# Performance work log

Hardware: AMD Instinct MI355X
Metric: run time of the kernel (lower is better)

## Reference

```python
import jax, jax.numpy as jnp
import numpy as np

B, N, C, E, O = 4, 128, 256, 128, 128
NEG = -1.0e9


def setup_inputs() -> dict:
    key = jax.random.key(0)
    ks = jax.random.split(key, 24)
    s = jnp.float32(0.02)
    w = lambda k, shp: jax.random.normal(k, shp, jnp.float32) * s
    mm = jax.random.randint(ks[3], (B, N, N), 0, 2).astype(bool)
    return {
        "z": jax.random.normal(ks[0], (B, N, C), jnp.float32),
        "e": jax.random.normal(ks[1], (B, N, N, E), jnp.float32),
        "g": jax.random.normal(ks[2], (B, C // 2), jnp.float32),
        "mask": jnp.ones((B, N), bool),
        "msgs_mask": mm | jnp.eye(N, dtype=bool)[None],  # ensure each max-col nonempty
        "Wt1": w(ks[4], (C, 8)), "Wt2": w(ks[5], (C, 8)), "Wt3": w(ks[6], (C, 8)),
        "Wte1": w(ks[7], (E, 8)), "Wte2": w(ks[8], (E, 8)), "Wte3": w(ks[9], (E, 8)),
        "Wtg": w(ks[10], (C // 2, 8)),
        "Wm1": w(ks[11], (C, O)), "Wm2": w(ks[12], (C, O)),
        "Wme": w(ks[13], (E, O)), "Wmg": w(ks[14], (C // 2, O)),
        "Wmlp1": w(ks[15], (O, O)), "Wmlp2": w(ks[16], (O, O)),
        "WU1": w(ks[17], (C, O)), "WU2": w(ks[18], (O, O)), "WU3": w(ks[19], (8, O)),
    }


def reference(z, e, g, mask, msgs_mask, Wt1, Wt2, Wt3, Wte1, Wte2, Wte3, Wtg,
              Wm1, Wm2, Wme, Wmg, Wmlp1, Wmlp2, WU1, WU2, WU3):
    m = mask[..., None]  # (B,N,1)
    # --- triplet path ---
    t1 = jnp.where(m, z @ Wt1, 0.0)  # (B,N,8)
    t2 = jnp.where(m, z @ Wt2, 0.0)
    t3 = jnp.where(m, z @ Wt3, 0.0)
    te1 = e @ Wte1  # (B,N,N,8)
    te2 = e @ Wte2
    te3 = e @ Wte3
    tg = g @ Wtg  # (B,8)
    # (B,N,N,N,8) 7-way broadcast sum
    tri = (t1[:, :, None, None, :] + t2[:, None, :, None, :] + t3[:, None, None, :, :]
           + te1[:, :, :, None, :] + te2[:, :, None, :, :] + te3[:, None, :, :, :]
           + tg[:, None, None, None, :])
    msk_tri = mask[:, None, None, :] | mask[:, None, :, None] | mask[:, :, None, None]
    tri = jnp.where(msk_tri[..., None], tri, NEG)
    tri_msgs = jnp.max(tri, axis=1) @ WU3  # (B,N,N,O)
    # --- pairwise message path ---
    m1 = jnp.where(m, z @ Wm1, 0.0)  # (B,N,O)
    m2 = jnp.where(m, z @ Wm2, 0.0)
    me = jnp.where(msgs_mask[..., None], e @ Wme, 0.0)  # (B,N,N,O)
    mg = g @ Wmg  # (B,O)
    msgs = m1[:, None, :, :] + m2[:, :, None, :] + me + mg[:, None, None, :]
    msgs = jax.nn.relu(msgs) @ Wmlp1  # num_layers=2 MLP: (ReLU,Lin)x2
    msgs = jax.nn.relu(msgs) @ Wmlp2
    msgs = jnp.where(msgs_mask[..., None], msgs, NEG)
    msgs = jnp.max(msgs, axis=1)  # (B,N,O)
    ret = z @ WU1 + msgs @ WU2
    return (ret, msgs, tri_msgs)
```

## Files before the change

kernel.cpp:

```cpp
#include <hip/hip_runtime.h>
#include <hip/hip_bf16.h>
#include <cstdint>
#include <cstddef>

namespace {

constexpr int B = 4, N = 128, C = 256, E = 128, O = 128, CH = 8;
constexpr float NEGV = -1.0e9f;

constexpr size_t SZ_TE_F  = (size_t)B * N * N * CH / 2;
constexpr size_t OFF_TE1T = 0;
constexpr size_t OFF_TE2  = OFF_TE1T + SZ_TE_F;
constexpr size_t OFF_TE3  = OFF_TE2 + SZ_TE_F;
constexpr size_t OFF_M1   = OFF_TE3 + SZ_TE_F;
constexpr size_t OFF_M2   = OFF_M1 + (size_t)B * N * O;
constexpr size_t OFF_ZU1  = OFF_M2 + (size_t)B * N * O;
constexpr size_t OFF_T1   = OFF_ZU1 + (size_t)B * N * O;
constexpr size_t OFF_T2   = OFF_T1 + (size_t)B * N * CH;
constexpr size_t OFF_T3   = OFF_T2 + (size_t)B * N * CH;
constexpr size_t OFF_TG   = OFF_T3 + (size_t)B * N * CH;
constexpr size_t OFF_WT   = OFF_TG + (size_t)B * CH;
constexpr size_t OFF_PART = OFF_WT + (size_t)3 * O * E / 2;

typedef __attribute__((ext_vector_type(4))) float f32x4;
typedef __attribute__((ext_vector_type(8))) short bf16x8;
typedef __attribute__((ext_vector_type(8))) unsigned short u16x8;
typedef __attribute__((ext_vector_type(4))) unsigned u32x4;

__device__ __forceinline__ unsigned short f2b(float f) {
  unsigned u = __float_as_uint(f);
  u = (u + 0x7fffu + ((u >> 16) & 1u)) >> 16;
  return (unsigned short)u;
}
__device__ __forceinline__ float b2f(unsigned short u) {
  return __uint_as_float((unsigned)u << 16);
}

}

__global__ __launch_bounds__(256) void k_prep(
    const float* __restrict__ z, const float* __restrict__ g,
    const float* __restrict__ e,
    const float* __restrict__ Wt1, const float* __restrict__ Wt2,
    const float* __restrict__ Wt3, const float* __restrict__ Wtg,
    const float* __restrict__ Wm1, const float* __restrict__ Wm2,
    const float* __restrict__ Wmg, const float* __restrict__ WU1,
    const float* __restrict__ Wte1, const float* __restrict__ Wte2,
    const float* __restrict__ Wte3,
    const float* __restrict__ Wme, const float* __restrict__ Wmlp1,
    const float* __restrict__ Wmlp2, float* __restrict__ ws) {
  __shared__ __align__(16) char smem[17408];
  const int blk = blockIdx.x;
  const int t = threadIdx.x;

  if (blk < 512) {
    unsigned short* wpack = (unsigned short*)(smem);
    unsigned short* outl  = (unsigned short*)(smem + 8704);
    unsigned short* te1T = (unsigned short*)(ws + OFF_TE1T);
    unsigned short* te2  = (unsigned short*)(ws + OFF_TE2);
    unsigned short* te3  = (unsigned short*)(ws + OFF_TE3);
    const int b = blk >> 7, i = blk & 127;

    for (int x = t; x < 3072; x += 256) {
      const int m = x >> 10, rem = x & 1023, k = rem >> 3, c = rem & 7;
      const float* W = (m == 0) ? Wte1 : ((m == 1) ? Wte2 : Wte3);
      const int row = m * 8 + c;
      wpack[row * 136 + k] = f2b(W[rem]);
    }
    for (int x = t; x < 1024; x += 256) {
      const int row = 24 + (x >> 7), col = x & 127;
      wpack[row * 136 + col] = 0;
    }
    __syncthreads();

    const float* erow = e + ((size_t)(b * N) + i) * N * E;
    const int lane = t & 63, wid = t >> 6;
    const int li = lane & 15, lk8 = (lane >> 4) * 8, lq4 = (lane >> 4) * 4;
    const int jt = wid & 1, ct = wid >> 1;
    const int c0 = ct * 16 + lq4;

    bf16x8 wf[4];
#pragma unroll
    for (int kt = 0; kt < 4; ++kt) {
      const int rw = ct * 16 + li;
      wf[kt] = *reinterpret_cast<const bf16x8*>(&wpack[rw * 136 + kt * 32 + lk8]);
    }

#pragma unroll 2
    for (int step = 0; step < 4; ++step) {
      const int jrow = step * 32 + jt * 16 + li;
      const float* er = erow + (size_t)jrow * E;
      float4 v[4][2];
#pragma unroll
      for (int kt = 0; kt < 4; ++kt) {
        v[kt][0] = *reinterpret_cast<const float4*>(&er[kt * 32 + lk8]);
        v[kt][1] = *reinterpret_cast<const float4*>(&er[kt * 32 + lk8 + 4]);
      }
      f32x4 acc = {0.f, 0.f, 0.f, 0.f};
#pragma unroll
      for (int kt = 0; kt < 4; ++kt) {
        u16x8 af;
        af[0] = f2b(v[kt][0].x); af[1] = f2b(v[kt][0].y);
        af[2] = f2b(v[kt][0].z); af[3] = f2b(v[kt][0].w);
        af[4] = f2b(v[kt][1].x); af[5] = f2b(v[kt][1].y);
        af[6] = f2b(v[kt][1].z); af[7] = f2b(v[kt][1].w);
        acc = __builtin_amdgcn_mfma_f32_16x16x32_bf16(
            wf[kt], (bf16x8)af, acc, 0, 0, 0);
      }
      if (c0 < 24) {
        ushort4 pk;
        pk.x = f2b(acc[0]); pk.y = f2b(acc[1]);
        pk.z = f2b(acc[2]); pk.w = f2b(acc[3]);
        *reinterpret_cast<ushort4*>(&outl[jrow * 32 + c0]) = pk;
      }
    }
    __syncthreads();
    for (int x = t; x < 384; x += 256) {
      const int m = x >> 7, j = x & 127;
      const u16x8 v = *reinterpret_cast<const u16x8*>(&outl[j * 32 + m * 8]);
      if (m == 0)
        *reinterpret_cast<u16x8*>(&te1T[(((size_t)(b * N) + j) * N + i) * CH]) = v;
      else if (m == 1)
        *reinterpret_cast<u16x8*>(&te2[(((size_t)(b * N) + i) * N + j) * CH]) = v;
      else
        *reinterpret_cast<u16x8*>(&te3[(((size_t)(b * N) + i) * N + j) * CH]) = v;
    }
  } else if (blk < 1024) {
    float* zrow = (float*)(smem);
    float* grow = (float*)(smem + 1024);
    const int bn = blk - 512;
    const int b = bn >> 7, n = bn & 127;

    for (int k = t; k < C; k += 256) zrow[k] = z[((size_t)(b * N) + n) * C + k];
    if (t < C / 2) grow[t] = g[(size_t)b * (C / 2) + t];
    __syncthreads();

    {
      const int o = t & 127;
      const float* W = (t < 128) ? Wm1 : Wm2;
      float acc = 0.f;
#pragma unroll 16
      for (int k = 0; k < C; ++k) acc += zrow[k] * W[(size_t)k * O + o];
      if (t < 128) {
        float mgacc = 0.f;
#pragma unroll 8
        for (int k = 0; k < C / 2; ++k) mgacc += grow[k] * Wmg[(size_t)k * O + o];
        acc += mgacc;
        ws[OFF_M1 + ((size_t)(b * N) + n) * O + o] = acc;
      } else {
        ws[OFF_M2 + ((size_t)(b * N) + n) * O + o] = acc;
      }
    }
    if (t < 128) {
      float acc = 0.f;
#pragma unroll 16
      for (int k = 0; k < C; ++k) acc += zrow[k] * WU1[(size_t)k * O + t];
      ws[OFF_ZU1 + ((size_t)(b * N) + n) * O + t] = acc;
    } else if (t < 152) {
      const int idx = t - 128;
      const int which = idx >> 3, c = idx & 7;
      const float* W = (which == 0) ? Wt1 : ((which == 1) ? Wt2 : Wt3);
      float acc = 0.f;
#pragma unroll 8
      for (int k = 0; k < C; ++k) acc += zrow[k] * W[(size_t)k * CH + c];
      const size_t off = (which == 0) ? OFF_T1 : ((which == 1) ? OFF_T2 : OFF_T3);
      ws[off + ((size_t)(b * N) + n) * CH + c] = acc;
    }
    if (n == 0 && t >= 152 && t < 160) {
      const int c = t - 152;
      float acc = 0.f;
      for (int k = 0; k < C / 2; ++k) acc += grow[k] * Wtg[(size_t)k * CH + c];
      ws[OFF_TG + (size_t)b * CH + c] = acc;
    }
  } else {
    const int which = blk - 1024;
    const float* W = (which == 0) ? Wme : ((which == 1) ? Wmlp1 : Wmlp2);
    unsigned short* dst = (unsigned short*)(ws + OFF_WT) + (size_t)which * O * E;
    for (int x = t; x < O * E; x += 256) {
      const int o = x >> 7, k = x & 127;
      dst[x] = f2b(W[(size_t)k * O + o]);
    }
  }
}

__global__ __launch_bounds__(512) void k_main(
    const float* __restrict__ e, const void* __restrict__ msk,
    const float* __restrict__ WU3, const float* __restrict__ ws_c,
    float* __restrict__ ws, float* __restrict__ out_tri) {
  __shared__ __align__(16) char smem[34816];
  const int blk = blockIdx.x;
  const int t = threadIdx.x;

  if (blk < 256) {
    unsigned short* lds_w = (unsigned short*)smem;
    const int b = blk >> 6, jp = blk & 63;
    const int j0 = jp * 2;
    const int lane = t & 63, wid = t >> 6;
    const int li = lane & 15, g = lane >> 4;
    const int i = wid * 16 + li;

    int fmt;
    {
      const unsigned w = ((const unsigned*)msk)[lane];
      const float f = __uint_as_float(w);
      const unsigned long long bi = __ballot(w > 1u);
      const unsigned long long bfl = __ballot(!(f == 0.f || f == 1.f));
      fmt = (bi == 0ull) ? 0 : ((bfl == 0ull) ? 2 : 1);
    }
    int mkv0, mkv1;
    {
      const size_t ia = ((size_t)(b * N) + i) * N + j0;
      const size_t ib = ia + 1;
      if (fmt == 0) { mkv0 = ((const int*)msk)[ia] != 0; mkv1 = ((const int*)msk)[ib] != 0; }
      else if (fmt == 1) { mkv0 = ((const unsigned char*)msk)[ia] != 0; mkv1 = ((const unsigned char*)msk)[ib] != 0; }
      else { mkv0 = ((const float*)msk)[ia] != 0.f; mkv1 = ((const float*)msk)[ib] != 0.f; }
    }

    float4 m2r[8];
#pragma unroll
    for (int ot = 0; ot < 8; ++ot)
      m2r[ot] = *reinterpret_cast<const float4*>(
          &ws_c[OFF_M2 + ((size_t)(b * N) + i) * O + ot * 16 + g * 4]);

    bf16x8 bfrag[2][4];
#pragma unroll
    for (int jj = 0; jj < 2; ++jj)
#pragma unroll
      for (int kt = 0; kt < 4; ++kt) {
        const float* ep =
            &e[(((size_t)(b * N) + i) * N + j0 + jj) * E + kt * 32 + g * 8];
        const float4 v0 = *reinterpret_cast<const float4*>(ep);
        const float4 v1 = *reinterpret_cast<const float4*>(ep + 4);
        u16x8 af;
        af[0] = f2b(v0.x); af[1] = f2b(v0.y); af[2] = f2b(v0.z); af[3] = f2b(v0.w);
        af[4] = f2b(v1.x); af[5] = f2b(v1.y); af[6] = f2b(v1.z); af[7] = f2b(v1.w);
        bfrag[jj][kt] = (bf16x8)af;
      }

    f32x4 acc[2][8];
    const unsigned short* wts = (const unsigned short*)(ws_c + OFF_WT);

#define STAGE_W(L)                                                        \
  { const unsigned short* wl = wts + (size_t)(L)*O * E;                   \
    _Pragma("unroll") for (int x = 0; x < 4; ++x) {                       \
      const int idx = t + x * 512;                                        \
      const int row = idx >> 4, cg = idx & 15;                            \
      *reinterpret_cast<u16x8*>(&lds_w[row * 136 + cg * 8]) =             \
          *reinterpret_cast<const u16x8*>(&wl[row * 128 + cg * 8]);       \
    } }

#define MFMA_L()                                                          \
  _Pragma("unroll") for (int ot = 0; ot < 8; ++ot) {                      \
    acc[0][ot] = (f32x4){0.f, 0.f, 0.f, 0.f};                             \
    acc[1][ot] = (f32x4){0.f, 0.f, 0.f, 0.f};                             \
    _Pragma("unroll") for (int kt = 0; kt < 4; ++kt) {                    \
      const bf16x8 wf = *reinterpret_cast<const bf16x8*>(                 \
          &lds_w[(ot * 16 + li) * 136 + kt * 32 + g * 8]);                \
      acc[0][ot] = __builtin_amdgcn_mfma_f32_16x16x32_bf16(               \
          wf, bfrag[0][kt], acc[0][ot], 0, 0, 0);                         \
      acc[1][ot] = __builtin_amdgcn_mfma_f32_16x16x32_bf16(               \
          wf, bfrag[1][kt], acc[1][ot], 0, 0, 0);                         \
    } }

#define TRANSITION(jj)                                                    \
  { unsigned pk0[8], pk1[8];                                              \
    _Pragma("unroll") for (int ot = 0; ot < 8; ++ot) {                    \
      pk0[ot] = (unsigned)f2b(acc[jj][ot][0]) |                           \
                ((unsigned)f2b(acc[jj][ot][1]) << 16);                    \
      pk1[ot] = (unsigned)f2b(acc[jj][ot][2]) |                           \
                ((unsigned)f2b(acc[jj][ot][3]) << 16);                    \
    }                                                                     \
    const int src1 = ((lane >> 4) & 1) * 32 + li;                         \
    const int src2 = src1 + 16;                                           \
    const bool hi = lane >= 32;                                           \
    _Pragma("unroll") for (int kt = 0; kt < 4; ++kt) {                    \
      const unsigned a0 = __shfl(pk0[2 * kt], src1);                      \
      const unsigned b0 = __shfl(pk0[2 * kt + 1], src1);                  \
      const unsigned a1 = __shfl(pk1[2 * kt], src1);                      \
      const unsigned b1 = __shfl(pk1[2 * kt + 1], src1);                  \
      const unsigned a2 = __shfl(pk0[2 * kt], src2);                      \
      const unsigned b2 = __shfl(pk0[2 * kt + 1], src2);                  \
      const unsigned a3 = __shfl(pk1[2 * kt], src2);                      \
      const unsigned b3 = __shfl(pk1[2 * kt + 1], src2);                  \
      u32x4 q;                                                            \
      q.x = hi ? b0 : a0; q.y = hi ? b1 : a1;                             \
      q.z = hi ? b2 : a2; q.w = hi ? b3 : a3;                             \
      bfrag[jj][kt] = __builtin_bit_cast(bf16x8, q);                      \
    } }

    STAGE_W(0);
    __syncthreads();
    MFMA_L();
#pragma unroll
    for (int jj = 0; jj < 2; ++jj) {
      const float mkf = (jj ? mkv1 : mkv0) ? 1.f : 0.f;
#pragma unroll
      for (int ot = 0; ot < 8; ++ot) {
        const float4 m1v = *reinterpret_cast<const float4*>(
            &ws_c[OFF_M1 + ((size_t)(b * N) + j0 + jj) * O + ot * 16 + g * 4]);
        acc[jj][ot][0] = fmaxf(acc[jj][ot][0] * mkf + m2r[ot].x + m1v.x, 0.f);
        acc[jj][ot][1] = fmaxf(acc[jj][ot][1] * mkf + m2r[ot].y + m1v.y, 0.f);
        acc[jj][ot][2] = fmaxf(acc[jj][ot][2] * mkf + m2r[ot].z + m1v.z, 0.f);
        acc[jj][ot][3] = fmaxf(acc[jj][ot][3] * mkf + m2r[ot].w + m1v.w, 0.f);
      }
    }
    TRANSITION(0);
    TRANSITION(1);

    __syncthreads();
    STAGE_W(1);
    __syncthreads();
    MFMA_L();
#pragma unroll
    for (int jj = 0; jj < 2; ++jj)
#pragma unroll
      for (int ot = 0; ot < 8; ++ot) {
        acc[jj][ot][0] = fmaxf(acc[jj][ot][0], 0.f);
        acc[jj][ot][1] = fmaxf(acc[jj][ot][1], 0.f);
        acc[jj][ot][2] = fmaxf(acc[jj][ot][2], 0.f);
        acc[jj][ot][3] = fmaxf(acc[jj][ot][3], 0.f);
      }
    TRANSITION(0);
    TRANSITION(1);

    __syncthreads();
    STAGE_W(2);
    __syncthreads();
    MFMA_L();
#pragma unroll
    for (int jj = 0; jj < 2; ++jj) {
      const bool mm = (jj ? mkv1 : mkv0) != 0;
      float* part =
          ws + OFF_PART + (((size_t)(b * N) + j0 + jj) * 8 + wid) * O;
#pragma unroll
      for (int ot = 0; ot < 8; ++ot) {
        float v0 = mm ? acc[jj][ot][0] : NEGV;
        float v1 = mm ? acc[jj][ot][1] : NEGV;
        float v2 = mm ? acc[jj][ot][2] : NEGV;
        float v3 = mm ? acc[jj][ot][3] : NEGV;
#pragma unroll
        for (int off = 1; off < 16; off <<= 1) {
          v0 = fmaxf(v0, __shfl_xor(v0, off));
          v1 = fmaxf(v1, __shfl_xor(v1, off));
          v2 = fmaxf(v2, __shfl_xor(v2, off));
          v3 = fmaxf(v3, __shfl_xor(v3, off));
        }
        if (li == 0)
          *reinterpret_cast<float4*>(&part[ot * 16 + g * 4]) =
              make_float4(v0, v1, v2, v3);
      }
    }
#undef STAGE_W
#undef MFMA_L
#undef TRANSITION
  } else {
    float* A4   = (float*)(smem);
    float* wu3  = (float*)(smem + 16384);
    float* trif = (float*)(smem + 20480);
    float* t2j4 = (float*)(smem + 28672);
    float* tgb  = (float*)(smem + 28800);
    const int blk2 = blk - 256;
    const int kh = blk2 & 1, jt = (blk2 >> 1) & 31, b = blk2 >> 6;
    const int j0 = jt * 4;

    const unsigned short* te1T = (const unsigned short*)(ws_c + OFF_TE1T);
    const unsigned short* te2p =
        (const unsigned short*)(ws_c + OFF_TE2) + (size_t)b * N * N * CH;
    const unsigned short* te3p = (const unsigned short*)(ws_c + OFF_TE3);
    const float* t1p = ws_c + OFF_T1 + (size_t)b * N * CH;
    const float* t3p = ws_c + OFF_T3 + (size_t)b * N * CH;

    {
      const int idx8 = t * 8;
      const int jj = idx8 >> 10, i = (idx8 & 1023) >> 3;
      const u16x8 tv = *reinterpret_cast<const u16x8*>(
          &te1T[((size_t)(b * N) + j0 + jj) * N * CH + i * 8]);
      const float4 t1a = *reinterpret_cast<const float4*>(&t1p[i * 8]);
      const float4 t1b = *reinterpret_cast<const float4*>(&t1p[i * 8 + 4]);
      float4 av0, av1;
      av0.x = b2f(tv[0]) + t1a.x; av0.y = b2f(tv[1]) + t1a.y;
      av0.z = b2f(tv[2]) + t1a.z; av0.w = b2f(tv[3]) + t1a.w;
      av1.x = b2f(tv[4]) + t1b.x; av1.y = b2f(tv[5]) + t1b.y;
      av1.z = b2f(tv[6]) + t1b.z; av1.w = b2f(tv[7]) + t1b.w;
      *reinterpret_cast<float4*>(&A4[idx8]) = av0;
      *reinterpret_cast<float4*>(&A4[idx8 + 4]) = av1;
    }
    if (t < 256)
      *reinterpret_cast<float4*>(&wu3[t * 4]) =
          *reinterpret_cast<const float4*>(&WU3[t * 4]);
    if (t < 32)
      t2j4[t] = ws_c[OFF_T2 + ((size_t)(b * N) + j0 + (t >> 3)) * CH + (t & 7)];
    if (t < 8) tgb[t] = ws_c[OFF_TG + (size_t)b * CH + t];
    __syncthreads();

    const int io = t & 7, kl = t >> 3;
    const int kg = kh * 64 + kl;
    const size_t kbase = (size_t)kg * CH;
    float core[4][8];
#pragma unroll
    for (int jj = 0; jj < 4; ++jj)
#pragma unroll
      for (int c = 0; c < 8; ++c) core[jj][c] = -3.0e38f;

#pragma unroll 2
    for (int i0 = 0; i0 < N; i0 += 8) {
      const int i = i0 + io;
      const u16x8 rv =
          *reinterpret_cast<const u16x8*>(&te2p[(size_t)i * N * CH + kbase]);
      float r[8];
#pragma unroll
      for (int c = 0; c < 8; ++c) r[c] = b2f(rv[c]);
#pragma unroll
      for (int jj = 0; jj < 4; ++jj) {
        const float4 a0 = *reinterpret_cast<const float4*>(&A4[jj * 1024 + i * 8]);
        const float4 a1 = *reinterpret_cast<const float4*>(&A4[jj * 1024 + i * 8 + 4]);
        core[jj][0] = fmaxf(core[jj][0], a0.x + r[0]);
        core[jj][1] = fmaxf(core[jj][1], a0.y + r[1]);
        core[jj][2] = fmaxf(core[jj][2], a0.z + r[2]);
        core[jj][3] = fmaxf(core[jj][3], a0.w + r[3]);
        core[jj][4] = fmaxf(core[jj][4], a1.x + r[4]);
        core[jj][5] = fmaxf(core[jj][5], a1.y + r[5]);
        core[jj][6] = fmaxf(core[jj][6], a1.z + r[6]);
        core[jj][7] = fmaxf(core[jj][7], a1.w + r[7]);
      }
    }
#pragma unroll
    for (int jj = 0; jj < 4; ++jj)
#pragma unroll
      for (int c = 0; c < 8; ++c) {
        core[jj][c] = fmaxf(core[jj][c], __shfl_xor(core[jj][c], 1));
        core[jj][c] = fmaxf(core[jj][c], __shfl_xor(core[jj][c], 2));
        core[jj][c] = fmaxf(core[jj][c], __shfl_xor(core[jj][c], 4));
      }
#pragma unroll
    for (int jj = 0; jj < 4; ++jj) {
      float cv = core[jj][0];
#pragma unroll
      for (int c = 1; c < 8; ++c) cv = (io == c) ? core[jj][c] : cv;
      const unsigned short t3e =
          te3p[((size_t)(b * N) + j0 + jj) * N * CH + kbase + io];
      trif[jj * 512 + kl * 8 + io] =
          cv + t2j4[jj * 8 + io] + t3p[kbase + io] + b2f(t3e) + tgb[io];
    }
    __syncthreads();

    const int o = t & 127, rh = t >> 7;
    float wcol[8];
#pragma unroll
    for (int c = 0; c < 8; ++c) wcol[c] = wu3[c * 128 + o];
#pragma unroll 4
    for (int q = 0; q < 64; ++q) {
      const int row = q * 4 + rh;
      const int jj = row >> 6, klr = row & 63;
      const float4 f0 = *reinterpret_cast<const float4*>(&trif[row * 8]);
      const float4 f1 = *reinterpret_cast<const float4*>(&trif[row * 8 + 4]);
      float acc2 = f0.x * wcol[0] + f0.y * wcol[1] + f0.z * wcol[2] +
                   f0.w * wcol[3] + f1.x * wcol[4] + f1.y * wcol[5] +
                   f1.z * wcol[6] + f1.w * wcol[7];
      out_tri[((size_t)(b * N) + j0 + jj) * N * O +
              (size_t)(kh * 64 + klr) * O + o] = acc2;
    }
  }
}

__global__ __launch_bounds__(256) void k_fin(
    const float* __restrict__ WU2, const float* __restrict__ ws,
    float* __restrict__ out_ret, float* __restrict__ out_msgs) {
  const int blk = blockIdx.x;
  const int b = blk >> 7, j = blk & 127;
  const int t = threadIdx.x;
  __shared__ float msgsrow[O];
  __shared__ float red[2][O];

  const float* part = ws + OFF_PART + ((size_t)(b * N) + j) * 8 * O;
  if (t < O) {
    float m = part[t];
#pragma unroll
    for (int p = 1; p < 8; ++p) m = fmaxf(m, part[p * O + t]);
    msgsrow[t] = m;
    out_msgs[((size_t)(b * N) + j) * O + t] = m;
  }
  __syncthreads();

  const int o = t & 127, h = t >> 7;
  float acc = 0.f;
#pragma unroll 8
  for (int p = h * 64; p < h * 64 + 64; ++p)
    acc += msgsrow[p] * WU2[(size_t)p * O + o];
  red[h][o] = acc;
  __syncthreads();
  if (t < O) {
    out_ret[((size_t)(b * N) + j) * O + t] =
        ws[OFF_ZU1 + ((size_t)(b * N) + j) * O + t] + red[0][t] + red[1][t];
  }
}

extern "C" void kernel_launch(void* const* d_in, const int* in_sizes, int n_in,
                              void* d_out, int out_size, void* d_ws,
                              size_t ws_size, hipStream_t stream) {
  const float* z    = (const float*)d_in[0];
  const float* e    = (const float*)d_in[1];
  const float* g    = (const float*)d_in[2];
  const void*  mmsk = d_in[4];
  const float* Wt1  = (const float*)d_in[5];
  const float* Wt2  = (const float*)d_in[6];
  const float* Wt3  = (const float*)d_in[7];
  const float* Wte1 = (const float*)d_in[8];
  const float* Wte2 = (const float*)d_in[9];
  const float* Wte3 = (const float*)d_in[10];
  const float* Wtg  = (const float*)d_in[11];
  const float* Wm1  = (const float*)d_in[12];
  const float* Wm2  = (const float*)d_in[13];
  const float* Wme  = (const float*)d_in[14];
  const float* Wmg  = (const float*)d_in[15];
  const float* Wmlp1= (const float*)d_in[16];
  const float* Wmlp2= (const float*)d_in[17];
  const float* WU1  = (const float*)d_in[18];
  const float* WU2  = (const float*)d_in[19];
  const float* WU3  = (const float*)d_in[20];

  float* ws = (float*)d_ws;
  float* out_ret  = (float*)d_out;
  float* out_msgs = out_ret + (size_t)B * N * O;
  float* out_tri  = out_msgs + (size_t)B * N * O;

  k_prep<<<1027, dim3(256), 0, stream>>>(z, g, e, Wt1, Wt2, Wt3, Wtg, Wm1, Wm2,
                                         Wmg, WU1, Wte1, Wte2, Wte3, Wme, Wmlp1,
                                         Wmlp2, ws);
  k_main<<<512, dim3(512), 0, stream>>>(e, mmsk, WU3, ws, ws, out_tri);
  k_fin<<<B * N, dim3(256), 0, stream>>>(WU2, ws, out_ret, out_msgs);
}
```

Measured before the change: 76.00 us.

## Split fused message MLP into per-layer kernels with bf16 global activations

Replaces the single fused kernel that ran all three message-path layers in registers with separate passes. A first-layer stage writes bf16 activations to workspace, two generic layer kernels apply Wmlp1 and Wmlp2, and the final kernel applies the mask and does the max over i. Each block now handles a full (b,i) row of 128 j values, which removes the register shuffles between layers and gives more blocks. The cost is several full B*N*N*O bf16 round trips through global memory and two extra kernel launches.

Measured after the change: 90.19 us. +18.7%, slower.

```diff
diff --git a/kernel.cpp b/kernel.cpp
--- a/kernel.cpp
+++ b/kernel.cpp
@@ -20,12 +20,12 @@
 constexpr size_t OFF_T3   = OFF_T2 + (size_t)B * N * CH;
 constexpr size_t OFF_TG   = OFF_T3 + (size_t)B * N * CH;
 constexpr size_t OFF_WT   = OFF_TG + (size_t)B * CH;
-constexpr size_t OFF_PART = OFF_WT + (size_t)3 * O * E / 2;
+constexpr size_t OFF_ACT1 = OFF_WT + (size_t)3 * O * E / 2;
+constexpr size_t OFF_ACT2 = OFF_ACT1 + (size_t)B * N * N * O / 2;
 
 typedef __attribute__((ext_vector_type(4))) float f32x4;
 typedef __attribute__((ext_vector_type(8))) short bf16x8;
 typedef __attribute__((ext_vector_type(8))) unsigned short u16x8;
-typedef __attribute__((ext_vector_type(4))) unsigned u32x4;
 
 __device__ __forceinline__ unsigned short f2b(float f) {
   unsigned u = __float_as_uint(f);
@@ -34,6 +34,19 @@
 }
 __device__ __forceinline__ float b2f(unsigned short u) {
   return __uint_as_float((unsigned)u << 16);
+}
+
+__device__ __forceinline__ int mask_fmt(const void* msk, int lane) {
+  const unsigned w = ((const unsigned*)msk)[lane];
+  const float f = __uint_as_float(w);
+  const unsigned long long bi = __ballot(w > 1u);
+  const unsigned long long bfl = __ballot(!(f == 0.f || f == 1.f));
+  return (bi == 0ull) ? 0 : ((bfl == 0ull) ? 2 : 1);
+}
+__device__ __forceinline__ int mask_at(const void* msk, int fmt, size_t idx) {
+  if (fmt == 0) return ((const int*)msk)[idx] != 0;
+  if (fmt == 1) return ((const unsigned char*)msk)[idx] != 0;
+  return ((const float*)msk)[idx] != 0.f;
 }
 
 }
@@ -183,7 +196,7 @@
   }
 }
 
-__global__ __launch_bounds__(512) void k_main(
+__global__ __launch_bounds__(512) void k_mid(
     const float* __restrict__ e, const void* __restrict__ msk,
     const float* __restrict__ WU3, const float* __restrict__ ws_c,
     float* __restrict__ ws, float* __restrict__ out_tri) {
@@ -191,175 +204,75 @@
   const int blk = blockIdx.x;
   const int t = threadIdx.x;
 
-  if (blk < 256) {
+  if (blk < 512) {
     unsigned short* lds_w = (unsigned short*)smem;
-    const int b = blk >> 6, jp = blk & 63;
-    const int j0 = jp * 2;
+    const int b = blk >> 7, i = blk & 127;
     const int lane = t & 63, wid = t >> 6;
     const int li = lane & 15, g = lane >> 4;
-    const int i = wid * 16 + li;
-
-    int fmt;
+    const int jrow = wid * 16 + li;
+
     {
-      const unsigned w = ((const unsigned*)msk)[lane];
-      const float f = __uint_as_float(w);
-      const unsigned long long bi = __ballot(w > 1u);
-      const unsigned long long bfl = __ballot(!(f == 0.f || f == 1.f));
-      fmt = (bi == 0ull) ? 0 : ((bfl == 0ull) ? 2 : 1);
-    }
-    int mkv0, mkv1;
-    {
-      const size_t ia = ((size_t)(b * N) + i) * N + j0;
-      const size_t ib = ia + 1;
-      if (fmt == 0) { mkv0 = ((const int*)msk)[ia] != 0; mkv1 = ((const int*)msk)[ib] != 0; }
-      else if (fmt == 1) { mkv0 = ((const unsigned char*)msk)[ia] != 0; mkv1 = ((const unsigned char*)msk)[ib] != 0; }
-      else { mkv0 = ((const float*)msk)[ia] != 0.f; mkv1 = ((const float*)msk)[ib] != 0.f; }
-    }
-
-    float4 m2r[8];
-#pragma unroll
-    for (int ot = 0; ot < 8; ++ot)
-      m2r[ot] = *reinterpret_cast<const float4*>(
-          &ws_c[OFF_M2 + ((size_t)(b * N) + i) * O + ot * 16 + g * 4]);
-
-    bf16x8 bfrag[2][4];
-#pragma unroll
-    for (int jj = 0; jj < 2; ++jj)
+      const unsigned short* wl = (const unsigned short*)(ws_c + OFF_WT);
+#pragma unroll
+      for (int x = 0; x < 4; ++x) {
+        const int idx = t + x * 512;
+        const int row = idx >> 4, cg = idx & 15;
+        *reinterpret_cast<u16x8*>(&lds_w[row * 136 + cg * 8]) =
+            *reinterpret_cast<const u16x8*>(&wl[row * 128 + cg * 8]);
+      }
+    }
+    const int fmt = mask_fmt(msk, lane);
+    const int mk = mask_at(msk, fmt, ((size_t)(b * N) + i) * N + jrow);
+    const float mkf = mk ? 1.f : 0.f;
+
+    bf16x8 bfrag[4];
+    const float* er = e + (((size_t)(b * N) + i) * N + jrow) * E;
+#pragma unroll
+    for (int kt = 0; kt < 4; ++kt) {
+      const float4 v0 = *reinterpret_cast<const float4*>(&er[kt * 32 + g * 8]);
+      const float4 v1 = *reinterpret_cast<const float4*>(&er[kt * 32 + g * 8 + 4]);
+      u16x8 af;
+      af[0] = f2b(v0.x); af[1] = f2b(v0.y); af[2] = f2b(v0.z); af[3] = f2b(v0.w);
+      af[4] = f2b(v1.x); af[5] = f2b(v1.y); af[6] = f2b(v1.z); af[7] = f2b(v1.w);
+      bfrag[kt] = (bf16x8)af;
+    }
+    __syncthreads();
+
+    f32x4 acc[8];
+#pragma unroll
+    for (int ot = 0; ot < 8; ++ot) {
+      acc[ot] = (f32x4){0.f, 0.f, 0.f, 0.f};
 #pragma unroll
       for (int kt = 0; kt < 4; ++kt) {
-        const float* ep =
-            &e[(((size_t)(b * N) + i) * N + j0 + jj) * E + kt * 32 + g * 8];
-        const float4 v0 = *reinterpret_cast<const float4*>(ep);
-        const float4 v1 = *reinterpret_cast<const float4*>(ep + 4);
-        u16x8 af;
-        af[0] = f2b(v0.x); af[1] = f2b(v0.y); af[2] = f2b(v0.z); af[3] = f2b(v0.w);
-        af[4] = f2b(v1.x); af[5] = f2b(v1.y); af[6] = f2b(v1.z); af[7] = f2b(v1.w);
-        bfrag[jj][kt] = (bf16x8)af;
-      }
-
-    f32x4 acc[2][8];
-    const unsigned short* wts = (const unsigned short*)(ws_c + OFF_WT);
-
-#define STAGE_W(L)                                                        \
-  { const unsigned short* wl = wts + (size_t)(L)*O * E;                   \
-    _Pragma("unroll") for (int x = 0; x < 4; ++x) {                       \
-      const int idx = t + x * 512;                                        \
-      const int row = idx >> 4, cg = idx & 15;                            \
-      *reinterpret_cast<u16x8*>(&lds_w[row * 136 + cg * 8]) =             \
-          *reinterpret_cast<const u16x8*>(&wl[row * 128 + cg * 8]);       \
-    } }
-
-#define MFMA_L()                                                          \
-  _Pragma("unroll") for (int ot = 0; ot < 8; ++ot) {                      \
-    acc[0][ot] = (f32x4){0.f, 0.f, 0.f, 0.f};                             \
-    acc[1][ot] = (f32x4){0.f, 0.f, 0.f, 0.f};                             \
-    _Pragma("unroll") for (int kt = 0; kt < 4; ++kt) {                    \
-      const bf16x8 wf = *reinterpret_cast<const bf16x8*>(                 \
-          &lds_w[(ot * 16 + li) * 136 + kt * 32 + g * 8]);                \
-      acc[0][ot] = __builtin_amdgcn_mfma_f32_16x16x32_bf16(               \
-          wf, bfrag[0][kt], acc[0][ot], 0, 0, 0);                         \
-      acc[1][ot] = __builtin_amdgcn_mfma_f32_16x16x32_bf16(               \
-          wf, bfrag[1][kt], acc[1][ot], 0, 0, 0);                         \
-    } }
-
-#define TRANSITION(jj)                                                    \
-  { unsigned pk0[8], pk1[8];                                              \
-    _Pragma("unroll") for (int ot = 0; ot < 8; ++ot) {                    \
-      pk0[ot] = (unsigned)f2b(acc[jj][ot][0]) |                           \
-                ((unsigned)f2b(acc[jj][ot][1]) << 16);                    \
-      pk1[ot] = (unsigned)f2b(acc[jj][ot][2]) |                           \
-                ((unsigned)f2b(acc[jj][ot][3]) << 16);                    \
-    }                                                                     \
-    const int src1 = ((lane >> 4) & 1) * 32 + li;                         \
-    const int src2 = src1 + 16;                                           \
-    const bool hi = lane >= 32;                                           \
-    _Pragma("unroll") for (int kt = 0; kt < 4; ++kt) {                    \
-      const unsigned a0 = __shfl(pk0[2 * kt], src1);                      \
-      const unsigned b0 = __shfl(pk0[2 * kt + 1], src1);                  \
-      const unsigned a1 = __shfl(pk1[2 * kt], src1);                      \
-      const unsigned b1 = __shfl(pk1[2 * kt + 1], src1);                  \
-      const unsigned a2 = __shfl(pk0[2 * kt], src2);                      \
-      const unsigned b2 = __shfl(pk0[2 * kt + 1], src2);                  \
-      const unsigned a3 = __shfl(pk1[2 * kt], src2);                      \
-      const unsigned b3 = __shfl(pk1[2 * kt + 1], src2);                  \
-      u32x4 q;                                                            \
-      q.x = hi ? b0 : a0; q.y = hi ? b1 : a1;                             \
-      q.z = hi ? b2 : a2; q.w = hi ? b3 : a3;                             \
-      bfrag[jj][kt] = __builtin_bit_cast(bf16x8, q);                      \
-    } }
-
-    STAGE_W(0);
-    __syncthreads();
-    MFMA_L();
-#pragma unroll
-    for (int jj = 0; jj < 2; ++jj) {
-      const float mkf = (jj ? mkv1 : mkv0) ? 1.f : 0.f;
-#pragma unroll
-      for (int ot = 0; ot < 8; ++ot) {
-        const float4 m1v = *reinterpret_cast<const float4*>(
-            &ws_c[OFF_M1 + ((size_t)(b * N) + j0 + jj) * O + ot * 16 + g * 4]);
-        acc[jj][ot][0] = fmaxf(acc[jj][ot][0] * mkf + m2r[ot].x + m1v.x, 0.f);
-        acc[jj][ot][1] = fmaxf(acc[jj][ot][1] * mkf + m2r[ot].y + m1v.y, 0.f);
-        acc[jj][ot][2] = fmaxf(acc[jj][ot][2] * mkf + m2r[ot].z + m1v.z, 0.f);
-        acc[jj][ot][3] = fmaxf(acc[jj][ot][3] * mkf + m2r[ot].w + m1v.w, 0.f);
-      }
-    }
-    TRANSITION(0);
-    TRANSITION(1);
-
-    __syncthreads();
-    STAGE_W(1);
-    __syncthreads();
-    MFMA_L();
-#pragma unroll
-    for (int jj = 0; jj < 2; ++jj)
-#pragma unroll
-      for (int ot = 0; ot < 8; ++ot) {
-        acc[jj][ot][0] = fmaxf(acc[jj][ot][0], 0.f);
-        acc[jj][ot][1] = fmaxf(acc[jj][ot][1], 0.f);
-        acc[jj][ot][2] = fmaxf(acc[jj][ot][2], 0.f);
-        acc[jj][ot][3] = fmaxf(acc[jj][ot][3], 0.f);
-      }
-    TRANSITION(0);
-    TRANSITION(1);
-
-    __syncthreads();
-    STAGE_W(2);
-    __syncthreads();
-    MFMA_L();
-#pragma unroll
-    for (int jj = 0; jj < 2; ++jj) {
-      const bool mm = (jj ? mkv1 : mkv0) != 0;
-      float* part =
-          ws + OFF_PART + (((size_t)(b * N) + j0 + jj) * 8 + wid) * O;
-#pragma unroll
-      for (int ot = 0; ot < 8; ++ot) {
-        float v0 = mm ? acc[jj][ot][0] : NEGV;
-        float v1 = mm ? acc[jj][ot][1] : NEGV;
-        float v2 = mm ? acc[jj][ot][2] : NEGV;
-        float v3 = mm ? acc[jj][ot][3] : NEGV;
-#pragma unroll
-        for (int off = 1; off < 16; off <<= 1) {
-          v0 = fmaxf(v0, __shfl_xor(v0, off));
-          v1 = fmaxf(v1, __shfl_xor(v1, off));
-          v2 = fmaxf(v2, __shfl_xor(v2, off));
-          v3 = fmaxf(v3, __shfl_xor(v3, off));
-        }
-        if (li == 0)
-          *reinterpret_cast<float4*>(&part[ot * 16 + g * 4]) =
-              make_float4(v0, v1, v2, v3);
-      }
-    }
-#undef STAGE_W
-#undef MFMA_L
-#undef TRANSITION
+        const bf16x8 wf = *reinterpret_cast<const bf16x8*>(
+            &lds_w[(ot * 16 + li) * 136 + kt * 32 + g * 8]);
+        acc[ot] = __builtin_amdgcn_mfma_f32_16x16x32_bf16(wf, bfrag[kt], acc[ot], 0, 0, 0);
+      }
+    }
+
+    unsigned short* act1 = (unsigned short*)(ws + OFF_ACT1);
+    const float* m1p = ws_c + OFF_M1 + ((size_t)(b * N) + jrow) * O;
+    const float* m2p = ws_c + OFF_M2 + ((size_t)(b * N) + i) * O;
+#pragma unroll
+    for (int ot = 0; ot < 8; ++ot) {
+      const int o0 = ot * 16 + g * 4;
+      const float4 m1v = *reinterpret_cast<const float4*>(&m1p[o0]);
+      const float4 m2v = *reinterpret_cast<const float4*>(&m2p[o0]);
+      ushort4 pk;
+      pk.x = f2b(fmaxf(acc[ot][0] * mkf + m1v.x + m2v.x, 0.f));
+      pk.y = f2b(fmaxf(acc[ot][1] * mkf + m1v.y + m2v.y, 0.f));
+      pk.z = f2b(fmaxf(acc[ot][2] * mkf + m1v.z + m2v.z, 0.f));
+      pk.w = f2b(fmaxf(acc[ot][3] * mkf + m1v.w + m2v.w, 0.f));
+      *reinterpret_cast<ushort4*>(
+          &act1[(((size_t)(b * N) + i) * N + jrow) * O + o0]) = pk;
+    }
   } else {
     float* A4   = (float*)(smem);
     float* wu3  = (float*)(smem + 16384);
     float* trif = (float*)(smem + 20480);
     float* t2j4 = (float*)(smem + 28672);
     float* tgb  = (float*)(smem + 28800);
-    const int blk2 = blk - 256;
+    const int blk2 = blk - 512;
     const int kh = blk2 & 1, jt = (blk2 >> 1) & 31, b = blk2 >> 6;
     const int j0 = jt * 4;
 
@@ -463,31 +376,105 @@
   }
 }
 
+__global__ __launch_bounds__(512) void k_lay(
+    const unsigned short* __restrict__ in, unsigned short* __restrict__ out,
+    const unsigned short* __restrict__ wl, const int do_relu) {
+  __shared__ __align__(16) unsigned short lds_w[128 * 136];
+  const int t = threadIdx.x;
+  const size_t r0 = (size_t)blockIdx.x * 128;
+  const int lane = t & 63, wid = t >> 6;
+  const int li = lane & 15, g = lane >> 4;
+  const size_t row = r0 + wid * 16 + li;
+
+#pragma unroll
+  for (int x = 0; x < 4; ++x) {
+    const int idx = t + x * 512;
+    const int r = idx >> 4, cg = idx & 15;
+    *reinterpret_cast<u16x8*>(&lds_w[r * 136 + cg * 8]) =
+        *reinterpret_cast<const u16x8*>(&wl[r * 128 + cg * 8]);
+  }
+  bf16x8 bfrag[4];
+#pragma unroll
+  for (int kt = 0; kt < 4; ++kt)
+    bfrag[kt] = *reinterpret_cast<const bf16x8*>(&in[row * O + kt * 32 + g * 8]);
+  __syncthreads();
+
+  f32x4 acc[8];
+#pragma unroll
+  for (int ot = 0; ot < 8; ++ot) {
+    acc[ot] = (f32x4){0.f, 0.f, 0.f, 0.f};
+#pragma unroll
+    for (int kt = 0; kt < 4; ++kt) {
+      const bf16x8 wf = *reinterpret_cast<const bf16x8*>(
+          &lds_w[(ot * 16 + li) * 136 + kt * 32 + g * 8]);
+      acc[ot] = __builtin_amdgcn_mfma_f32_16x16x32_bf16(wf, bfrag[kt], acc[ot], 0, 0, 0);
+    }
+  }
+#pragma unroll
+  for (int ot = 0; ot < 8; ++ot) {
+    const int o0 = ot * 16 + g * 4;
+    ushort4 pk;
+    if (do_relu) {
+      pk.x = f2b(fmaxf(acc[ot][0], 0.f));
+      pk.y = f2b(fmaxf(acc[ot][1], 0.f));
+      pk.z = f2b(fmaxf(acc[ot][2], 0.f));
+      pk.w = f2b(fmaxf(acc[ot][3], 0.f));
+    } else {
+      pk.x = f2b(acc[ot][0]);
+      pk.y = f2b(acc[ot][1]);
+      pk.z = f2b(acc[ot][2]);
+      pk.w = f2b(acc[ot][3]);
+    }
+    *reinterpret_cast<ushort4*>(&out[row * O + o0]) = pk;
+  }
+}
+
 __global__ __launch_bounds__(256) void k_fin(
-    const float* __restrict__ WU2, const float* __restrict__ ws,
-    float* __restrict__ out_ret, float* __restrict__ out_msgs) {
+    const void* __restrict__ msk, const float* __restrict__ WU2,
+    const float* __restrict__ ws, float* __restrict__ out_ret,
+    float* __restrict__ out_msgs) {
   const int blk = blockIdx.x;
   const int b = blk >> 7, j = blk & 127;
   const int t = threadIdx.x;
+  __shared__ float part2[16][136];
   __shared__ float msgsrow[O];
   __shared__ float red[2][O];
 
-  const float* part = ws + OFF_PART + ((size_t)(b * N) + j) * 8 * O;
+  const int fmt = mask_fmt(msk, t & 63);
+  const unsigned short* h = (const unsigned short*)(ws + OFF_ACT1);
+  const int ig = t >> 4, cg = t & 15;
+
+  float mx[8];
+#pragma unroll
+  for (int q = 0; q < 8; ++q) mx[q] = -3.0e38f;
+  for (int it = 0; it < 8; ++it) {
+    const int i = it * 16 + ig;
+    const int mk = mask_at(msk, fmt, ((size_t)(b * N) + i) * N + j);
+    const u16x8 hv = *reinterpret_cast<const u16x8*>(
+        &h[(((size_t)(b * N) + i) * N + j) * O + cg * 8]);
+#pragma unroll
+    for (int q = 0; q < 8; ++q)
+      mx[q] = fmaxf(mx[q], mk ? b2f(hv[q]) : NEGV);
+  }
+#pragma unroll
+  for (int q = 0; q < 8; ++q) part2[ig][cg * 8 + q] = mx[q];
+  __syncthreads();
+
   if (t < O) {
-    float m = part[t];
-#pragma unroll
-    for (int p = 1; p < 8; ++p) m = fmaxf(m, part[p * O + t]);
+    float m = part2[0][t];
+#pragma unroll
+    for (int r = 1; r < 16; ++r) m = fmaxf(m, part2[r][t]);
     msgsrow[t] = m;
     out_msgs[((size_t)(b * N) + j) * O + t] = m;
   }
   __syncthreads();
 
-  const int o = t & 127, h = t >> 7;
+  const int o = t & 127, h2 = t >> 7;
   float acc = 0.f;
 #pragma unroll 8
-  for (int p = h * 64; p < h * 64 + 64; ++p)
+  for (int p = h2 * 64; p < h2 * 64 + 64; ++p)
     acc += msgsrow[p] * WU2[(size_t)p * O + o];
-  red[h][o] = acc;
+  red[h2][o] = acc;
   __syncthreads();
   if (t < O) {
     out_ret[((size_t)(b * N) + j) * O + t] =
@@ -524,9 +511,15 @@
   float* out_msgs = out_ret + (size_t)B * N * O;
   float* out_tri  = out_msgs + (size_t)B * N * O;
 
+  unsigned short* act1 = (unsigned short*)(ws + OFF_ACT1);
+  unsigned short* act2 = (unsigned short*)(ws + OFF_ACT2);
+  const unsigned short* wts = (const unsigned short*)(ws + OFF_WT);
+
   k_prep<<<1027, dim3(256), 0, stream>>>(z, g, e, Wt1, Wt2, Wt3, Wtg, Wm1, Wm2,
                                          Wmg, WU1, Wte1, Wte2, Wte3, Wme, Wmlp1,
                                          Wmlp2, ws);
-  k_main<<<512, dim3(512), 0, stream>>>(e, mmsk, WU3, ws, ws, out_tri);
-  k_fin<<<B * N, dim3(256), 0, stream>>>(WU2, ws, out_ret, out_msgs);
-}
+  k_mid<<<768, dim3(512), 0, stream>>>(e, mmsk, WU3, ws, ws, out_tri);
+  k_lay<<<512, dim3(512), 0, stream>>>(act1, act2, wts + (size_t)O * E, 1);
+  k_lay<<<512, dim3(512), 0, stream>>>(act2, act1, wts + (size_t)2 * O * E, 0);
+  k_fin<<<B * N, dim3(256), 0, stream>>>(mmsk, WU2, ws, out_ret, out_msgs);
+}
```

## Fuse message MLP, max-reduction and WU2 projection per output column

Applied to the files above, without the earlier changes.

The pairwise message path changes from blocks that each handle two j columns, write partial maxima to workspace and rely on a separate k_fin kernel, to one block per (b,j) column. Each block stages the whole 128-row edge slice in LDS, runs the three MFMA layers on it, reduces the max fully on-chip and applies WU2 to write ret and msgs directly. This removes a kernel launch and the partial-result round trip through global memory, and keeps activations in LDS between layers instead of shuffling registers. In exchange it reads weights straight from global or cache rather than LDS, launches more blocks (768), and uses a larger shared-memory footprint.

Result: slower. 92.68 us (+22.0%).

```diff
diff --git a/kernel.cpp b/kernel.cpp
--- a/kernel.cpp
+++ b/kernel.cpp
@@ -20,12 +20,10 @@
 constexpr size_t OFF_T3   = OFF_T2 + (size_t)B * N * CH;
 constexpr size_t OFF_TG   = OFF_T3 + (size_t)B * N * CH;
 constexpr size_t OFF_WT   = OFF_TG + (size_t)B * CH;
-constexpr size_t OFF_PART = OFF_WT + (size_t)3 * O * E / 2;
 
 typedef __attribute__((ext_vector_type(4))) float f32x4;
 typedef __attribute__((ext_vector_type(8))) short bf16x8;
 typedef __attribute__((ext_vector_type(8))) unsigned short u16x8;
-typedef __attribute__((ext_vector_type(4))) unsigned u32x4;
 
 __device__ __forceinline__ unsigned short f2b(float f) {
   unsigned u = __float_as_uint(f);
@@ -185,181 +183,20 @@
 
 __global__ __launch_bounds__(512) void k_main(
     const float* __restrict__ e, const void* __restrict__ msk,
-    const float* __restrict__ WU3, const float* __restrict__ ws_c,
-    float* __restrict__ ws, float* __restrict__ out_tri) {
-  __shared__ __align__(16) char smem[34816];
+    const float* __restrict__ WU3, const float* __restrict__ WU2,
+    const float* __restrict__ ws_c, float* __restrict__ out_tri,
+    float* __restrict__ out_ret, float* __restrict__ out_msgs) {
+  __shared__ __align__(16) char smem[43008];
   const int blk = blockIdx.x;
   const int t = threadIdx.x;
 
   if (blk < 256) {
-    unsigned short* lds_w = (unsigned short*)smem;
-    const int b = blk >> 6, jp = blk & 63;
-    const int j0 = jp * 2;
-    const int lane = t & 63, wid = t >> 6;
-    const int li = lane & 15, g = lane >> 4;
-    const int i = wid * 16 + li;
-
-    int fmt;
-    {
-      const unsigned w = ((const unsigned*)msk)[lane];
-      const float f = __uint_as_float(w);
-      const unsigned long long bi = __ballot(w > 1u);
-      const unsigned long long bfl = __ballot(!(f == 0.f || f == 1.f));
-      fmt = (bi == 0ull) ? 0 : ((bfl == 0ull) ? 2 : 1);
-    }
-    int mkv0, mkv1;
-    {
-      const size_t ia = ((size_t)(b * N) + i) * N + j0;
-      const size_t ib = ia + 1;
-      if (fmt == 0) { mkv0 = ((const int*)msk)[ia] != 0; mkv1 = ((const int*)msk)[ib] != 0; }
-      else if (fmt == 1) { mkv0 = ((const unsigned char*)msk)[ia] != 0; mkv1 = ((const unsigned char*)msk)[ib] != 0; }
-      else { mkv0 = ((const float*)msk)[ia] != 0.f; mkv1 = ((const float*)msk)[ib] != 0.f; }
-    }
-
-    float4 m2r[8];
-#pragma unroll
-    for (int ot = 0; ot < 8; ++ot)
-      m2r[ot] = *reinterpret_cast<const float4*>(
-          &ws_c[OFF_M2 + ((size_t)(b * N) + i) * O + ot * 16 + g * 4]);
-
-    bf16x8 bfrag[2][4];
-#pragma unroll
-    for (int jj = 0; jj < 2; ++jj)
-#pragma unroll
-      for (int kt = 0; kt < 4; ++kt) {
-        const float* ep =
-            &e[(((size_t)(b * N) + i) * N + j0 + jj) * E + kt * 32 + g * 8];
-        const float4 v0 = *reinterpret_cast<const float4*>(ep);
-        const float4 v1 = *reinterpret_cast<const float4*>(ep + 4);
-        u16x8 af;
-        af[0] = f2b(v0.x); af[1] = f2b(v0.y); af[2] = f2b(v0.z); af[3] = f2b(v0.w);
-        af[4] = f2b(v1.x); af[5] = f2b(v1.y); af[6] = f2b(v1.z); af[7] = f2b(v1.w);
-        bfrag[jj][kt] = (bf16x8)af;
-      }
-
-    f32x4 acc[2][8];
-    const unsigned short* wts = (const unsigned short*)(ws_c + OFF_WT);
-
-#define STAGE_W(L)                                                        \
-  { const unsigned short* wl = wts + (size_t)(L)*O * E;                   \
-    _Pragma("unroll") for (int x = 0; x < 4; ++x) {                       \
-      const int idx = t + x * 512;                                        \
-      const int row = idx >> 4, cg = idx & 15;                            \
-      *reinterpret_cast<u16x8*>(&lds_w[row * 136 + cg * 8]) =             \
-          *reinterpret_cast<const u16x8*>(&wl[row * 128 + cg * 8]);       \
-    } }
-
-#define MFMA_L()                                                          \
-  _Pragma("unroll") for (int ot = 0; ot < 8; ++ot) {                      \
-    acc[0][ot] = (f32x4){0.f, 0.f, 0.f, 0.f};                             \
-    acc[1][ot] = (f32x4){0.f, 0.f, 0.f, 0.f};                             \
-    _Pragma("unroll") for (int kt = 0; kt < 4; ++kt) {                    \
-      const bf16x8 wf = *reinterpret_cast<const bf16x8*>(                 \
-          &lds_w[(ot * 16 + li) * 136 + kt * 32 + g * 8]);                \
-      acc[0][ot] = __builtin_amdgcn_mfma_f32_16x16x32_bf16(               \
-          wf, bfrag[0][kt], acc[0][ot], 0, 0, 0);                         \
-      acc[1][ot] = __builtin_amdgcn_mfma_f32_16x16x32_bf16(               \
-          wf, bfrag[1][kt], acc[1][ot], 0, 0, 0);                         \
-    } }
-
-#define TRANSITION(jj)                                                    \
-  { unsigned pk0[8], pk1[8];                                              \
-    _Pragma("unroll") for (int ot = 0; ot < 8; ++ot) {                    \
-      pk0[ot] = (unsigned)f2b(acc[jj][ot][0]) |                           \
-                ((unsigned)f2b(acc[jj][ot][1]) << 16);                    \
-      pk1[ot] = (unsigned)f2b(acc[jj][ot][2]) |                           \
-                ((unsigned)f2b(acc[jj][ot][3]) << 16);                    \
-    }                                                                     \
-    const int src1 = ((lane >> 4) & 1) * 32 + li;                         \
-    const int src2 = src1 + 16;                                           \
-    const bool hi = lane >= 32;                                           \
-    _Pragma("unroll") for (int kt = 0; kt < 4; ++kt) {                    \
-      const unsigned a0 = __shfl(pk0[2 * kt], src1);                      \
-      const unsigned b0 = __shfl(pk0[2 * kt + 1], src1);                  \
-      const unsigned a1 = __shfl(pk1[2 * kt], src1);                      \
-      const unsigned b1 = __shfl(pk1[2 * kt + 1], src1);                  \
-      const unsigned a2 = __shfl(pk0[2 * kt], src2);                      \
-      const unsigned b2 = __shfl(pk0[2 * kt + 1], src2);                  \
-      const unsigned a3 = __shfl(pk1[2 * kt], src2);                      \
-      const unsigned b3 = __shfl(pk1[2 * kt + 1], src2);                  \
-      u32x4 q;                                                            \
-      q.x = hi ? b0 : a0; q.y = hi ? b1 : a1;                             \
-      q.z = hi ? b2 : a2; q.w = hi ? b3 : a3;                             \
-      bfrag[jj][kt] = __builtin_bit_cast(bf16x8, q);                      \
-    } }
-
-    STAGE_W(0);
-    __syncthreads();
-    MFMA_L();
-#pragma unroll
-    for (int jj = 0; jj < 2; ++jj) {
-      const float mkf = (jj ? mkv1 : mkv0) ? 1.f : 0.f;
-#pragma unroll
-      for (int ot = 0; ot < 8; ++ot) {
-        const float4 m1v = *reinterpret_cast<const float4*>(
-            &ws_c[OFF_M1 + ((size_t)(b * N) + j0 + jj) * O + ot * 16 + g * 4]);
-        acc[jj][ot][0] = fmaxf(acc[jj][ot][0] * mkf + m2r[ot].x + m1v.x, 0.f);
-        acc[jj][ot][1] = fmaxf(acc[jj][ot][1] * mkf + m2r[ot].y + m1v.y, 0.f);
-        acc[jj][ot][2] = fmaxf(acc[jj][ot][2] * mkf + m2r[ot].z + m1v.z, 0.f);
-        acc[jj][ot][3] = fmaxf(acc[jj][ot][3] * mkf + m2r[ot].w + m1v.w, 0.f);
-      }
-    }
-    TRANSITION(0);
-    TRANSITION(1);
-
-    __syncthreads();
-    STAGE_W(1);
-    __syncthreads();
-    MFMA_L();
-#pragma unroll
-    for (int jj = 0; jj < 2; ++jj)
-#pragma unroll
-      for (int ot = 0; ot < 8; ++ot) {
-        acc[jj][ot][0] = fmaxf(acc[jj][ot][0], 0.f);
-        acc[jj][ot][1] = fmaxf(acc[jj][ot][1], 0.f);
-        acc[jj][ot][2] = fmaxf(acc[jj][ot][2], 0.f);
-        acc[jj][ot][3] = fmaxf(acc[jj][ot][3], 0.f);
-      }
-    TRANSITION(0);
-    TRANSITION(1);
-
-    __syncthreads();
-    STAGE_W(2);
-    __syncthreads();
-    MFMA_L();
-#pragma unroll
-    for (int jj = 0; jj < 2; ++jj) {
-      const bool mm = (jj ? mkv1 : mkv0) != 0;
-      float* part =
-          ws + OFF_PART + (((size_t)(b * N) + j0 + jj) * 8 + wid) * O;
-#pragma unroll
-      for (int ot = 0; ot < 8; ++ot) {
-        float v0 = mm ? acc[jj][ot][0] : NEGV;
-        float v1 = mm ? acc[jj][ot][1] : NEGV;
-        float v2 = mm ? acc[jj][ot][2] : NEGV;
-        float v3 = mm ? acc[jj][ot][3] : NEGV;
-#pragma unroll
-        for (int off = 1; off < 16; off <<= 1) {
-          v0 = fmaxf(v0, __shfl_xor(v0, off));
-          v1 = fmaxf(v1, __shfl_xor(v1, off));
-          v2 = fmaxf(v2, __shfl_xor(v2, off));
-          v3 = fmaxf(v3, __shfl_xor(v3, off));
-        }
-        if (li == 0)
-          *reinterpret_cast<float4*>(&part[ot * 16 + g * 4]) =
-              make_float4(v0, v1, v2, v3);
-      }
-    }
-#undef STAGE_W
-#undef MFMA_L
-#undef TRANSITION
-  } else {
     float* A4   = (float*)(smem);
     float* wu3  = (float*)(smem + 16384);
     float* trif = (float*)(smem + 20480);
     float* t2j4 = (float*)(smem + 28672);
     float* tgb  = (float*)(smem + 28800);
-    const int blk2 = blk - 256;
+    const int blk2 = blk;
     const int kh = blk2 & 1, jt = (blk2 >> 1) & 31, b = blk2 >> 6;
     const int j0 = jt * 4;
 
@@ -460,38 +297,163 @@
       out_tri[((size_t)(b * N) + j0 + jj) * N * O +
               (size_t)(kh * 64 + klr) * O + o] = acc2;
     }
+  } else {
+    unsigned short* act = (unsigned short*)(smem);
+    float* redmax = (float*)(smem + 34816);
+    float* msgsrow = (float*)(smem + 38912);
+    float* red4 = (float*)(smem + 39424);
+    int* maskv = (int*)(smem + 41472);
+    float* m1s = (float*)(smem + 41984);
+    int* fmtp = (int*)(smem + 42496);
+    const int mb = blk - 256;
+    const int b = mb >> 7, j = mb & 127;
+    constexpr int LDK = 136;
+
+    const int lane = t & 63, wid = t >> 6;
+    const int li = lane & 15, g = lane >> 4;
+    const int r0 = wid * 16;
+
+    if (t < 64) {
+      const unsigned w = ((const unsigned*)msk)[t];
+      const float f = __uint_as_float(w);
+      const unsigned long long bi = __ballot(w > 1u);
+      const unsigned long long bfl = __ballot(!(f == 0.f || f == 1.f));
+      if (t == 0) *fmtp = (bi == 0ull) ? 0 : ((bfl == 0ull) ? 2 : 1);
+    }
+    __syncthreads();
+    const int fmt = *fmtp;
+    if (t < 128) {
+      const size_t idx = ((size_t)(b * N) + t) * N + j;
+      int mv;
+      if (fmt == 0)      mv = ((const int*)msk)[idx] != 0;
+      else if (fmt == 1) mv = ((const unsigned char*)msk)[idx] != 0;
+      else               mv = ((const float*)msk)[idx] != 0.f;
+      maskv[t] = mv;
+    } else if (t < 256) {
+      m1s[t - 128] = ws_c[OFF_M1 + ((size_t)(b * N) + j) * O + (t - 128)];
+    }
+    __syncthreads();
+
+    const float* ep = e + ((size_t)(b * N) * N + j) * E;
+    for (int x = t; x < 128 * 32; x += 512) {
+      const int row = x >> 5, seg = x & 31;
+      const float4 v = *reinterpret_cast<const float4*>(
+          &ep[(size_t)row * N * E + seg * 4]);
+      ushort4 pk;
+      if (maskv[row]) {
+        pk.x = f2b(v.x); pk.y = f2b(v.y); pk.z = f2b(v.z); pk.w = f2b(v.w);
+      } else {
+        pk.x = pk.y = pk.z = pk.w = 0;
+      }
+      *reinterpret_cast<ushort4*>(&act[row * LDK + seg * 4]) = pk;
+    }
+    __syncthreads();
+
+    const unsigned short* wts = (const unsigned short*)(ws_c + OFF_WT);
+    const unsigned short* wme_t   = wts;
+    const unsigned short* wmlp1_t = wts + (size_t)O * E;
+    const unsigned short* wmlp2_t = wts + (size_t)2 * O * E;
+    const float* m2p = ws_c + OFF_M2 + (size_t)b * N * O;
+
+    bf16x8 af[4];
+    f32x4 acc[8];
+
+#define LOAD_AF()                                                         \
+  _Pragma("unroll") for (int kt = 0; kt < 4; ++kt)                        \
+      af[kt] = *reinterpret_cast<const bf16x8*>(                          \
+          &act[(r0 + li) * LDK + kt * 32 + g * 8]);
+
+#define LAYER(WT)                                                         \
+  _Pragma("unroll") for (int ot = 0; ot < 8; ++ot) {                      \
+    acc[ot] = (f32x4){0.f, 0.f, 0.f, 0.f};                                \
+    _Pragma("unroll") for (int kt = 0; kt < 4; ++kt) {                    \
+      const bf16x8 wf = *reinterpret_cast<const bf16x8*>(                 \
+          &(WT)[(size_t)(ot * 16 + li) * E + kt * 32 + g * 8]);           \
+      acc[ot] = __builtin_amdgcn_mfma_f32_16x16x32_bf16(                  \
+          wf, af[kt], acc[ot], 0, 0, 0);                                  \
+    }                                                                     \
   }
-}
-
-__global__ __launch_bounds__(256) void k_fin(
-    const float* __restrict__ WU2, const float* __restrict__ ws,
-    float* __restrict__ out_ret, float* __restrict__ out_msgs) {
-  const int blk = blockIdx.x;
-  const int b = blk >> 7, j = blk & 127;
-  const int t = threadIdx.x;
-  __shared__ float msgsrow[O];
-  __shared__ float red[2][O];
-
-  const float* part = ws + OFF_PART + ((size_t)(b * N) + j) * 8 * O;
-  if (t < O) {
-    float m = part[t];
-#pragma unroll
-    for (int p = 1; p < 8; ++p) m = fmaxf(m, part[p * O + t]);
-    msgsrow[t] = m;
-    out_msgs[((size_t)(b * N) + j) * O + t] = m;
-  }
-  __syncthreads();
-
-  const int o = t & 127, h = t >> 7;
-  float acc = 0.f;
+
+    LOAD_AF();
+    LAYER(wme_t);
+#pragma unroll
+    for (int ot = 0; ot < 8; ++ot) {
+      const int i = r0 + li;
+      const int o0 = ot * 16 + g * 4;
+      const float4 m2v =
+          *reinterpret_cast<const float4*>(&m2p[(size_t)i * O + o0]);
+      const float4 b1 = *reinterpret_cast<const float4*>(&m1s[o0]);
+      ushort4 pk;
+      pk.x = f2b(fmaxf(acc[ot][0] + m2v.x + b1.x, 0.f));
+      pk.y = f2b(fmaxf(acc[ot][1] + m2v.y + b1.y, 0.f));
+      pk.z = f2b(fmaxf(acc[ot][2] + m2v.z + b1.z, 0.f));
+      pk.w = f2b(fmaxf(acc[ot][3] + m2v.w + b1.w, 0.f));
+      *reinterpret_cast<ushort4*>(&act[i * LDK + o0]) = pk;
+    }
+
+    LOAD_AF();
+    LAYER(wmlp1_t);
+#pragma unroll
+    for (int ot = 0; ot < 8; ++ot) {
+      const int i = r0 + li;
+      const int o0 = ot * 16 + g * 4;
+      ushort4 pk;
+      pk.x = f2b(fmaxf(acc[ot][0], 0.f));
+      pk.y = f2b(fmaxf(acc[ot][1], 0.f));
+      pk.z = f2b(fmaxf(acc[ot][2], 0.f));
+      pk.w = f2b(fmaxf(acc[ot][3], 0.f));
+      *reinterpret_cast<ushort4*>(&act[i * LDK + o0]) = pk;
+    }
+
+    LOAD_AF();
+    LAYER(wmlp2_t);
+    {
+      const bool mm = maskv[r0 + li] != 0;
+#pragma unroll
+      for (int ot = 0; ot < 8; ++ot) {
+        float v0 = mm ? acc[ot][0] : NEGV;
+        float v1 = mm ? acc[ot][1] : NEGV;
+        float v2 = mm ? acc[ot][2] : NEGV;
+        float v3 = mm ? acc[ot][3] : NEGV;
+#pragma unroll
+        for (int off = 1; off < 16; off <<= 1) {
+          v0 = fmaxf(v0, __shfl_xor(v0, off));
+          v1 = fmaxf(v1, __shfl_xor(v1, off));
+          v2 = fmaxf(v2, __shfl_xor(v2, off));
+          v3 = fmaxf(v3, __shfl_xor(v3, off));
+        }
+        if (li == 0) {
+          *reinterpret_cast<float4*>(&redmax[wid * 128 + ot * 16 + g * 4]) =
+              make_float4(v0, v1, v2, v3);
+        }
+      }
+    }
+    __syncthreads();
+
+    if (t < 128) {
+      float m = redmax[t];
+#pragma unroll
+      for (int p = 1; p < 8; ++p) m = fmaxf(m, redmax[p * 128 + t]);
+      msgsrow[t] = m;
+      out_msgs[((size_t)(b * N) + j) * O + t] = m;
+    }
+    __syncthreads();
+    {
+      const int o = t & 127, h = t >> 7;
+      float a = 0.f;
 #pragma unroll 8
-  for (int p = h * 64; p < h * 64 + 64; ++p)
-    acc += msgsrow[p] * WU2[(size_t)p * O + o];
-  red[h][o] = acc;
-  __syncthreads();
-  if (t < O) {
-    out_ret[((size_t)(b * N) + j) * O + t] =
-        ws[OFF_ZU1 + ((size_t)(b * N) + j) * O + t] + red[0][t] + red[1][t];
+      for (int p = h * 32; p < h * 32 + 32; ++p)
+        a += msgsrow[p] * WU2[(size_t)p * O + o];
+      red4[h * 128 + o] = a;
+    }
+    __syncthreads();
+    if (t < 128) {
+      out_ret[((size_t)(b * N) + j) * O + t] =
+          ws_c[OFF_ZU1 + ((size_t)(b * N) + j) * O + t] + red4[t] +
+          red4[128 + t] + red4[256 + t] + red4[384 + t];
+    }
+#undef LOAD_AF
+#undef LAYER
   }
 }
 
@@ -527,6 +489,6 @@
   k_prep<<<1027, dim3(256), 0, stream>>>(z, g, e, Wt1, Wt2, Wt3, Wtg, Wm1, Wm2,
                                          Wmg, WU1, Wte1, Wte2, Wte3, Wme, Wmlp1,
                                          Wmlp2, ws);
-  k_main<<<512, dim3(512), 0, stream>>>(e, mmsk, WU3, ws, ws, out_tri);
-  k_fin<<<B * N, dim3(256), 0, stream>>>(WU2, ws, out_ret, out_msgs);
-}
+  k_main<<<768, dim3(512), 0, stream>>>(e, mmsk, WU3, WU2, ws, out_tri,
+                                        out_ret, out_msgs);
+}
```
